# Performance work log

Hardware: AMD Instinct MI355X
Metric: run time of the kernel (lower is better)

The kernel has to match this reference:

```python
import jax, jax.numpy as jnp
import numpy as np

LATENT, CTX, HID, TDIM, HEADS = 512, 512, 1024, 128, 8
HEAD_DIM = HID // HEADS
SCALE = HEAD_DIM ** -0.5


def _ln(x, g, b, eps=1e-5):
    m = jnp.mean(x, axis=-1, keepdims=True)
    v = jnp.mean((x - m) ** 2, axis=-1, keepdims=True)
    return (x - m) * jax.lax.rsqrt(v + eps) * g + b


def _time_embed(t):
    half = TDIM // 2
    exponent = jnp.linspace(0.0, 1.0, half, dtype=t.dtype)
    freqs = jnp.exp(jnp.log(1000.0) * exponent)
    ang = 2.0 * jnp.pi * t[:, None] * freqs[None, :]
    return jnp.concatenate([jnp.sin(ang), jnp.cos(ang)], axis=-1)  # [B, TDIM]


def setup_inputs() -> dict:
    key = jax.random.key(0)
    ks = iter(jax.random.split(key, 32))
    B, M = 4096, 64

    def w(k, i, o):
        return jax.random.normal(k, (i, o), jnp.float32) * 0.02

    inp = {
        "states": jax.random.normal(next(ks), (B, LATENT), jnp.float32),
        "time_values": jax.random.uniform(next(ks), (B,), jnp.float32),
        "class_summary": jax.random.normal(next(ks), (B, CTX), jnp.float32),
        "support_memory": jax.random.normal(next(ks), (B, M, LATENT), jnp.float32),
        # state_trunk: LN(latent+tdim) -> Linear -> GELU -> Linear
        "trunk_ln_g": jnp.ones((LATENT + TDIM,)), "trunk_ln_b": jnp.zeros((LATENT + TDIM,)),
        "trunk_w1": w(next(ks), LATENT + TDIM, HID), "trunk_b1": jnp.zeros((HID,)),
        "trunk_w2": w(next(ks), HID, HID), "trunk_b2": jnp.zeros((HID,)),
        # memory adapter: LN(latent) -> Linear(latent, hid)
        "mem_ln_g": jnp.ones((LATENT,)), "mem_ln_b": jnp.zeros((LATENT,)),
        "mem_w": w(next(ks), LATENT, HID), "mem_b": jnp.zeros((HID,)),
        # attention projections
        "wq": w(next(ks), HID, HID), "bq": jnp.zeros((HID,)),
        "wk": w(next(ks), HID, HID), "bk": jnp.zeros((HID,)),
        "wv": w(next(ks), HID, HID), "bv": jnp.zeros((HID,)),
        "wo": w(next(ks), HID, HID), "bo": jnp.zeros((HID,)),
        # pre-condition norm + FiLM
        "pre_ln_g": jnp.ones((HID,)), "pre_ln_b": jnp.zeros((HID,)),
        "film_w": w(next(ks), CTX, 2 * HID), "film_b": jnp.zeros((2 * HID,)),
        # conditioner: LN -> Linear -> GELU -> Linear
        "cond_ln_g": jnp.ones((HID,)), "cond_ln_b": jnp.zeros((HID,)),
        "cond_w1": w(next(ks), HID, HID), "cond_b1": jnp.zeros((HID,)),
        "cond_w2": w(next(ks), HID, HID), "cond_b2": jnp.zeros((HID,)),
        # output head: LN -> Linear -> GELU -> Linear(hid, latent)
        "head_ln_g": jnp.ones((HID,)), "head_ln_b": jnp.zeros((HID,)),
        "head_w1": w(next(ks), HID, HID), "head_b1": jnp.zeros((HID,)),
        "head_w2": w(next(ks), HID, LATENT), "head_b2": jnp.zeros((LATENT,)),
    }
    return inp


def _forward(states, time_values, class_summary, support_memory,
             trunk_ln_g, trunk_ln_b, trunk_w1, trunk_b1, trunk_w2, trunk_b2,
             mem_ln_g, mem_ln_b, mem_w, mem_b,
             wq, bq, wk, bk, wv, bv, wo, bo,
             pre_ln_g, pre_ln_b, film_w, film_b,
             cond_ln_g, cond_ln_b, cond_w1, cond_b1, cond_w2, cond_b2,
             head_ln_g, head_ln_b, head_w1, head_b1, head_w2, head_b2):
    B, M, _ = support_memory.shape
    gelu = lambda x: jax.nn.gelu(x, approximate=False)

    # trunk: g = Trunk([y, gamma(t)])
    te = _time_embed(time_values)
    x = _ln(jnp.concatenate([states, te], axis=-1), trunk_ln_g, trunk_ln_b)
    g = gelu(x @ trunk_w1 + trunk_b1) @ trunk_w2 + trunk_b2  # [B, HID]

    # encode memory + single-query multi-head attention
    mem_h = _ln(support_memory, mem_ln_g, mem_ln_b) @ mem_w + mem_b  # [B, M, HID]
    q = (g @ wq + bq).reshape(B, HEADS, HEAD_DIM)
    k = (mem_h @ wk + bk).reshape(B, M, HEADS, HEAD_DIM)
    v = (mem_h @ wv + bv).reshape(B, M, HEADS, HEAD_DIM)
    logits = jnp.einsum("bhd,bmhd->bhm", q, k) * SCALE
    attn = jax.nn.softmax(logits, axis=-1)
    summary = jnp.einsum("bhm,bmhd->bhd", attn, v).reshape(B, HID)
    attn_summary = summary @ wo + bo

    # FiLM conditioning
    combined = _ln(g + attn_summary, pre_ln_g, pre_ln_b)
    film = class_summary @ film_w + film_b
    scale, shift = film[:, :HID], film[:, HID:]
    combined = (1.0 + scale) * combined + shift
    cond_x = _ln(combined, cond_ln_g, cond_ln_b)
    conditioned = gelu(cond_x @ cond_w1 + cond_b1) @ cond_w2 + cond_b2 + combined

    # output head
    hx = _ln(conditioned, head_ln_g, head_ln_b)
    return gelu(hx @ head_w1 + head_b1) @ head_w2 + head_b2  # [B, LATENT]


def reference(states, time_values, class_summary, support_memory,
              trunk_ln_g, trunk_ln_b, trunk_w1, trunk_b1, trunk_w2, trunk_b2,
              mem_ln_g, mem_ln_b, mem_w, mem_b,
              wq, bq, wk, bk, wv, bv, wo, bo,
              pre_ln_g, pre_ln_b, film_w, film_b,
              cond_ln_g, cond_ln_b, cond_w1, cond_b1, cond_w2, cond_b2,
              head_ln_g, head_ln_b, head_w1, head_b1, head_w2, head_b2):
    return _forward(states, time_values, class_summary, support_memory,
                    trunk_ln_g, trunk_ln_b, trunk_w1, trunk_b1, trunk_w2, trunk_b2,
                    mem_ln_g, mem_ln_b, mem_w, mem_b,
                    wq, bq, wk, bk, wv, bv, wo, bo,
                    pre_ln_g, pre_ln_b, film_w, film_b,
                    cond_ln_g, cond_ln_b, cond_w1, cond_b1, cond_w2, cond_b2,
                    head_ln_g, head_ln_b, head_w1, head_b1, head_w2, head_b2)
```

## Files before the change

### kernel.cpp

```cpp
#include <hip/hip_runtime.h>
#include <cstdint>
#include <cstddef>

typedef unsigned short ushort_t;
typedef short s16x8 __attribute__((ext_vector_type(8)));
typedef float f32x4 __attribute__((ext_vector_type(4)));

__device__ __forceinline__ float bf2f(ushort_t h){
  union { unsigned int u; float f; } v; v.u = ((unsigned int)h) << 16; return v.f;
}
__device__ __forceinline__ ushort_t f2bf(float x){
  union { float f; unsigned int u; } v; v.f = x;
  unsigned int r = v.u + 0x7FFFu + ((v.u >> 16) & 1u);
  return (ushort_t)(r >> 16);
}
__device__ __forceinline__ float gelu_f(float x){
  return 0.5f * x * (1.0f + erff(x * 0.7071067811865475f));
}
__device__ __forceinline__ float wave_sum(float v){
  #pragma unroll
  for (int o = 32; o; o >>= 1) v += __shfl_xor(v, o);
  return v;
}
__device__ __forceinline__ void block_reduce2(float& s, float& q, float* red){
  s = wave_sum(s); q = wave_sum(q);
  int w = threadIdx.x >> 6, lane = threadIdx.x & 63, nw = blockDim.x >> 6;
  if (lane == 0){ red[w] = s; red[8 + w] = q; }
  __syncthreads();
  float ts = 0.f, tq = 0.f;
  for (int i = 0; i < nw; ++i){ ts += red[i]; tq += red[8 + i]; }
  __syncthreads();
  s = ts; q = tq;
}

struct TDesc { const float* in; ushort_t* out; int K; int N; int start; };
struct PrepArgs {
  TDesc t[11];
  int ntiles_end;
  int cast1_blocks;
  int cast_end;
  const float* memw; ushort_t* memwb;
  const float* csum; ushort_t* csb;
  const float* memb; const float* wv; const float* bvp; float* bv2;
};

__global__ __launch_bounds__(256) void prep_k(PrepArgs a){
  int bid = blockIdx.x, tid = threadIdx.x;
  if (bid < a.ntiles_end){
    int d = 0;
    #pragma unroll
    for (int i = 1; i < 11; ++i) if (bid >= a.t[i].start) d = i;
    TDesc td = a.t[d];
    int tile = bid - td.start;
    int tilesx = td.N >> 5;
    int n0 = (tile % tilesx) << 5, k0 = (tile / tilesx) << 5;
    __shared__ float tbuf[32][33];
    int tx = tid & 31, ty = tid >> 5;
    #pragma unroll
    for (int j = 0; j < 32; j += 8)
      tbuf[ty + j][tx] = td.in[(size_t)(k0 + ty + j) * td.N + (n0 + tx)];
    __syncthreads();
    #pragma unroll
    for (int j = 0; j < 32; j += 8)
      td.out[(size_t)(n0 + ty + j) * td.K + (k0 + tx)] = f2bf(tbuf[tx][ty + j]);
  } else if (bid < a.cast_end){
    int ci = bid - a.ntiles_end;
    const float* src; ushort_t* dst; int i;
    if (ci < a.cast1_blocks){ src = a.memw; dst = a.memwb; i = ci * 1024 + tid * 4; }
    else { src = a.csum; dst = a.csb; i = (ci - a.cast1_blocks) * 1024 + tid * 4; }
    float4 v = *(const float4*)(src + i);
    union { ushort_t u[4]; uint2 p; } pk;
    pk.u[0] = f2bf(v.x); pk.u[1] = f2bf(v.y); pk.u[2] = f2bf(v.z); pk.u[3] = f2bf(v.w);
    *(uint2*)(dst + i) = pk.p;
  } else {
    int col = (bid - a.cast_end) * 256 + tid;
    float a0 = 0.f, a1 = 0.f, a2 = 0.f, a3 = 0.f;
    for (int j = 0; j < 1024; j += 4){
      a0 += a.memb[j + 0] * a.wv[(size_t)(j + 0) * 1024 + col];
      a1 += a.memb[j + 1] * a.wv[(size_t)(j + 1) * 1024 + col];
      a2 += a.memb[j + 2] * a.wv[(size_t)(j + 2) * 1024 + col];
      a3 += a.memb[j + 3] * a.wv[(size_t)(j + 3) * 1024 + col];
    }
    a.bv2[col] = a0 + a1 + a2 + a3 + a.bvp[col];
  }
}

__global__ __launch_bounds__(256) void ln_trunk_k(const float* __restrict__ states, const float* __restrict__ tv,
    const float* __restrict__ g, const float* __restrict__ b, ushort_t* __restrict__ out){
  int row = blockIdx.x, tid = threadIdx.x;
  __shared__ float buf[640];
  __shared__ float red[16];
  float t = tv[row];
  for (int i = tid; i < 640; i += 256){
    float v;
    if (i < 512) v = states[(size_t)row * 512 + i];
    else {
      int j = i - 512, jj = j & 63;
      float fr = expf(6.907755278982137f * ((float)jj * (1.0f / 63.0f)));
      float ang = 6.283185307179586f * t * fr;
      v = (j < 64) ? sinf(ang) : cosf(ang);
    }
    buf[i] = v;
  }
  __syncthreads();
  float s = 0.f, q = 0.f;
  for (int i = tid; i < 640; i += 256){ float v = buf[i]; s += v; q += v * v; }
  block_reduce2(s, q, red);
  float mean = s * (1.0f / 640.0f);
  float var = q * (1.0f / 640.0f) - mean * mean;
  float rstd = rsqrtf(var + 1e-5f);
  for (int i = tid; i < 640; i += 256)
    out[(size_t)row * 640 + i] = f2bf((buf[i] - mean) * rstd * g[i] + b[i]);
}

__global__ __launch_bounds__(256) void ln_rows_k(const float* __restrict__ in, const float* __restrict__ g,
    const float* __restrict__ b, ushort_t* __restrict__ out, int D){
  int row = blockIdx.x, tid = threadIdx.x, i = tid * 4;
  __shared__ float red[16];
  const float* x = in + (size_t)row * D;
  float4 v = *(const float4*)(x + i);
  float s = v.x + v.y + v.z + v.w;
  float q = v.x * v.x + v.y * v.y + v.z * v.z + v.w * v.w;
  block_reduce2(s, q, red);
  float invD = 1.0f / (float)D;
  float mean = s * invD, var = q * invD - mean * mean, rstd = rsqrtf(var + 1e-5f);
  union { ushort_t u[4]; uint2 p; } pk;
  pk.u[0] = f2bf((v.x - mean) * rstd * g[i + 0] + b[i + 0]);
  pk.u[1] = f2bf((v.y - mean) * rstd * g[i + 1] + b[i + 1]);
  pk.u[2] = f2bf((v.z - mean) * rstd * g[i + 2] + b[i + 2]);
  pk.u[3] = f2bf((v.w - mean) * rstd * g[i + 3] + b[i + 3]);
  *(uint2*)(out + (size_t)row * D + i) = pk.p;
}

__global__ __launch_bounds__(256) void fuse_film_k(const float* __restrict__ combf, const ushort_t* __restrict__ filmb,
    const float* __restrict__ pg, const float* __restrict__ pb,
    const float* __restrict__ cg, const float* __restrict__ cb,
    float* __restrict__ c2f, ushort_t* __restrict__ cxb){
  int row = blockIdx.x, tid = threadIdx.x, i = tid * 4;
  __shared__ float red[16];
  float4 a = *(const float4*)(combf + (size_t)row * 1024 + i);
  float x[4] = { a.x, a.y, a.z, a.w };
  float s = x[0] + x[1] + x[2] + x[3];
  float q = x[0]*x[0] + x[1]*x[1] + x[2]*x[2] + x[3]*x[3];
  block_reduce2(s, q, red);
  float mean = s * (1.0f / 1024.0f), var = q * (1.0f / 1024.0f) - mean * mean;
  float rstd = rsqrtf(var + 1e-5f);
  float4 pgv = *(const float4*)(pg + i), pbv = *(const float4*)(pb + i);
  union { uint2 p; ushort_t u[4]; } scv, shv;
  scv.p = *(const uint2*)(filmb + (size_t)row * 2048 + i);
  shv.p = *(const uint2*)(filmb + (size_t)row * 2048 + 1024 + i);
  float c2[4];
  {
    float pgx[4] = { pgv.x, pgv.y, pgv.z, pgv.w };
    float pbx[4] = { pbv.x, pbv.y, pbv.z, pbv.w };
    #pragma unroll
    for (int e = 0; e < 4; ++e){
      float cc = (x[e] - mean) * rstd * pgx[e] + pbx[e];
      c2[e] = (1.0f + bf2f(scv.u[e])) * cc + bf2f(shv.u[e]);
    }
  }
  *(float4*)(c2f + (size_t)row * 1024 + i) = make_float4(c2[0], c2[1], c2[2], c2[3]);
  float s2 = c2[0] + c2[1] + c2[2] + c2[3];
  float q2 = c2[0]*c2[0] + c2[1]*c2[1] + c2[2]*c2[2] + c2[3]*c2[3];
  block_reduce2(s2, q2, red);
  float m2 = s2 * (1.0f / 1024.0f), v2 = q2 * (1.0f / 1024.0f) - m2 * m2;
  float r2 = rsqrtf(v2 + 1e-5f);
  float4 cgv = *(const float4*)(cg + i), cbv = *(const float4*)(cb + i);
  union { ushort_t u[4]; uint2 p; } pk;
  pk.u[0] = f2bf((c2[0] - m2) * r2 * cgv.x + cbv.x);
  pk.u[1] = f2bf((c2[1] - m2) * r2 * cgv.y + cbv.y);
  pk.u[2] = f2bf((c2[2] - m2) * r2 * cgv.z + cbv.z);
  pk.u[3] = f2bf((c2[3] - m2) * r2 * cgv.w + cbv.w);
  *(uint2*)(cxb + (size_t)row * 1024 + i) = pk.p;
}

__global__ __launch_bounds__(256, 2) void suppattn_k(
    const float* __restrict__ support, const float* __restrict__ lgw, const float* __restrict__ lbw,
    const ushort_t* __restrict__ U, ushort_t* __restrict__ R)
{
  __shared__ ushort_t S[64 * 512];
  __shared__ ushort_t UG[9 * 512];
  __shared__ float WT[8][64];
  __shared__ float SUMV[64], SUMSQ[64];
  __shared__ __align__(16) float MEANR[64];
  __shared__ __align__(16) float RSTDR[64];
  __shared__ float PMAX[4][8], PSUM[4][8], PMU[4][8];
  __shared__ float AB[2][8];
  __shared__ float MUH[8];

  int bb = blockIdx.x, tid = threadIdx.x, w = tid >> 6, l = tid & 63;
  const ushort_t* Ub = U + (size_t)bb * 4096;

  for (int id = tid; id < 576; id += 256){
    int hr = id >> 6, cc = id & 63;
    int byteoff = hr * 1024 + (((cc & 56) | ((cc & 7) ^ (hr & 7))) << 4);
    uint4* dst = (uint4*)((char*)UG + byteoff);
    if (hr < 8){
      s16x8 uv = *(const s16x8*)(Ub + hr * 512 + cc * 8);
      float4 g0 = *(const float4*)(lgw + cc * 8);
      float4 g1 = *(const float4*)(lgw + cc * 8 + 4);
      float ga[8] = { g0.x, g0.y, g0.z, g0.w, g1.x, g1.y, g1.z, g1.w };
      union { ushort_t u[8]; uint4 p; } pk;
      #pragma unroll
      for (int e = 0; e < 8; ++e) pk.u[e] = f2bf(ga[e] * bf2f((ushort_t)uv[e]));
      *dst = pk.p;
    } else {
      *dst = make_uint4(0x3F803F80u, 0x3F803F80u, 0x3F803F80u, 0x3F803F80u);
    }
  }

  {
    int h0 = 2 * w, h1 = 2 * w + 1;
    s16x8 u0 = *(const s16x8*)(Ub + h0 * 512 + l * 8);
    s16x8 u1 = *(const s16x8*)(Ub + h1 * 512 + l * 8);
    float4 g0 = *(const float4*)(lgw + l * 8), g1 = *(const float4*)(lgw + l * 8 + 4);
    float4 c0 = *(const float4*)(lbw + l * 8), c1 = *(const float4*)(lbw + l * 8 + 4);
    float ga[8] = { g0.x, g0.y, g0.z, g0.w, g1.x, g1.y, g1.z, g1.w };
    float ba[8] = { c0.x, c0.y, c0.z, c0.w, c1.x, c1.y, c1.z, c1.w };
    float A0 = 0.f, B0 = 0.f, A1 = 0.f, B1 = 0.f;
    #pragma unroll
    for (int e = 0; e < 8; ++e){
      float x0 = bf2f((ushort_t)u0[e]), x1 = bf2f((ushort_t)u1[e]);
      A0 += ba[e] * x0; B0 += ga[e] * x0;
      A1 += ba[e] * x1; B1 += ga[e] * x1;
    }
    A0 = wave_sum(A0); B0 = wave_sum(B0); A1 = wave_sum(A1); B1 = wave_sum(B1);
    if (l == 0){ AB[0][h0] = A0; AB[1][h0] = B0; AB[0][h1] = A1; AB[1][h1] = B1; }
  }

  #pragma unroll 4
  for (int i = 0; i < 16; ++i){
    int m = i * 4 + w;
    const float* row = support + ((size_t)bb * 64 + m) * 512 + l * 8;
    float4 a0 = *(const float4*)row, a1 = *(const float4*)(row + 4);
    union { ushort_t u[8]; uint4 p; } pk;
    pk.u[0] = f2bf(a0.x); pk.u[1] = f2bf(a0.y); pk.u[2] = f2bf(a0.z); pk.u[3] = f2bf(a0.w);
    pk.u[4] = f2bf(a1.x); pk.u[5] = f2bf(a1.y); pk.u[6] = f2bf(a1.z); pk.u[7] = f2bf(a1.w);
    int byteoff = m * 1024 + (((l & 56) | ((l & 7) ^ (m & 7))) << 4);
    *(uint4*)((char*)S + byteoff) = pk.p;
  }
  __syncthreads();

  int l15 = l & 15, lk = l >> 4;
  int hr = (l15 < 8) ? l15 : 8;
  int arowb = (w * 16 + l15) * 1024;
  int hrowb = hr * 1024;
  f32x4 dacc = (f32x4){0.f, 0.f, 0.f, 0.f};
  f32x4 sacc = (f32x4){0.f, 0.f, 0.f, 0.f};
  #pragma unroll
  for (int ks = 0; ks < 16; ++ks){
    int cc = ks * 4 + lk;
    s16x8 afr = *(const s16x8*)((char*)S + arowb + (((cc & 56) | ((cc & 7) ^ (l15 & 7))) << 4));
    s16x8 bfr = *(const s16x8*)((char*)UG + hrowb + (((cc & 56) | ((cc & 7) ^ (hr & 7))) << 4));
    dacc = __builtin_amdgcn_mfma_f32_16x16x32_bf16(afr, bfr, dacc, 0, 0, 0);
    sacc = __builtin_amdgcn_mfma_f32_16x16x32_bf16(afr, afr, sacc, 0, 0, 0);
  }
  if (l15 == 8){
    #pragma unroll
    for (int j = 0; j < 4; ++j) SUMV[w * 16 + lk * 4 + j] = dacc[j];
  }
  if ((l15 >> 2) == lk) SUMSQ[w * 16 + l15] = sacc[l15 & 3];
  __syncthreads();
  if (tid < 64){
    float mean = SUMV[tid] * (1.0f / 512.0f);
    float var = SUMSQ[tid] * (1.0f / 512.0f) - mean * mean;
    MEANR[tid] = mean;
    RSTDR[tid] = rsqrtf(var + 1e-5f);
  }
  __syncthreads();

  int r0 = w * 16 + lk * 4;
  float4 mns = *(const float4*)(MEANR + r0);
  float4 rst = *(const float4*)(RSTDR + r0);
  float mn[4] = { mns.x, mns.y, mns.z, mns.w };
  float rs[4] = { rst.x, rst.y, rst.z, rst.w };
  float Ah = AB[0][l15 & 7], Bh = AB[1][l15 & 7];
  float lg[4];
  #pragma unroll
  for (int j = 0; j < 4; ++j)
    lg[j] = 0.08838834764831845f * (rs[j] * (dacc[j] - mn[j] * Bh) + Ah);
  float lmax = fmaxf(fmaxf(lg[0], lg[1]), fmaxf(lg[2], lg[3]));
  lmax = fmaxf(lmax, __shfl_xor(lmax, 16));
  lmax = fmaxf(lmax, __shfl_xor(lmax, 32));
  if (l < 8) PMAX[w][l] = lmax;
  __syncthreads();
  float gmax = fmaxf(fmaxf(PMAX[0][l15 & 7], PMAX[1][l15 & 7]),
                     fmaxf(PMAX[2][l15 & 7], PMAX[3][l15 & 7]));
  float e4[4]; float ls = 0.f, lm = 0.f;
  #pragma unroll
  for (int j = 0; j < 4; ++j){
    e4[j] = __expf(lg[j] - gmax);
    ls += e4[j];
    lm += e4[j] * rs[j] * mn[j];
  }
  ls += __shfl_xor(ls, 16); ls += __shfl_xor(ls, 32);
  lm += __shfl_xor(lm, 16); lm += __shfl_xor(lm, 32);
  if (l < 8){ PSUM[w][l] = ls; PMU[w][l] = lm; }
  __syncthreads();
  float Sh = PSUM[0][l15 & 7] + PSUM[1][l15 & 7] + PSUM[2][l15 & 7] + PSUM[3][l15 & 7];
  float inv = 1.0f / Sh;
  if (l15 < 8){
    #pragma unroll
    for (int j = 0; j < 4; ++j) WT[l15][r0 + j] = e4[j] * rs[j] * inv;
  }
  if (w == 0 && l < 8){
    MUH[l] = (PMU[0][l] + PMU[1][l] + PMU[2][l] + PMU[3][l]) * inv;
  }
  __syncthreads();

  int h0 = 2 * w, h1 = 2 * w + 1;
  float acc0[8] = {0.f,0.f,0.f,0.f,0.f,0.f,0.f,0.f};
  float acc1[8] = {0.f,0.f,0.f,0.f,0.f,0.f,0.f,0.f};
  #pragma unroll 4
  for (int m = 0; m < 64; ++m){
    s16x8 sv = *(const s16x8*)((char*)S + m * 1024 + (((l & 56) | ((l & 7) ^ (m & 7))) << 4));
    float f0 = WT[h0][m], f1 = WT[h1][m];
    #pragma unroll
    for (int e = 0; e < 8; ++e){
      float x = bf2f((ushort_t)sv[e]);
      acc0[e] += f0 * x;
      acc1[e] += f1 * x;
    }
  }
  {
    float4 g0 = *(const float4*)(lgw + l * 8), g1 = *(const float4*)(lgw + l * 8 + 4);
    float4 c0 = *(const float4*)(lbw + l * 8), c1 = *(const float4*)(lbw + l * 8 + 4);
    float ga[8] = { g0.x, g0.y, g0.z, g0.w, g1.x, g1.y, g1.z, g1.w };
    float ba[8] = { c0.x, c0.y, c0.z, c0.w, c1.x, c1.y, c1.z, c1.w };
    float mu0 = MUH[h0], mu1 = MUH[h1];
    union { ushort_t u[8]; uint4 p; } p0, p1;
    #pragma unroll
    for (int e = 0; e < 8; ++e){
      p0.u[e] = f2bf(ga[e] * (acc0[e] - mu0) + ba[e]);
      p1.u[e] = f2bf(ga[e] * (acc1[e] - mu1) + ba[e]);
    }
    *(uint4*)(R + (size_t)bb * 4096 + h0 * 512 + l * 8) = p0.p;
    *(uint4*)(R + (size_t)bb * 4096 + h1 * 512 + l * 8) = p1.p;
  }
}

#define GLL16(gsrc, ldst) \
  __builtin_amdgcn_global_load_lds((const __attribute__((address_space(1))) unsigned int*)(gsrc), \
                                   (__attribute__((address_space(3))) unsigned int*)(ldst), 16, 0, 0)

template<bool GELU, bool BIAS, bool WF32, bool WBF16, bool RESID>
__global__ __launch_bounds__(256, 3) void gemm_k(
    const ushort_t* __restrict__ A, int lda, long long aZ,
    const ushort_t* __restrict__ Bt, int ldb, long long bZ,
    const float* __restrict__ bias, long long biasZ,
    float* __restrict__ C, int ldc, long long cZ,
    ushort_t* __restrict__ Cb, int ldcb, long long cbZ,
    const float* __restrict__ R, int ldr,
    int M, int N, int K)
{
  __shared__ ushort_t smA[2][64 * 64];
  __shared__ ushort_t smB[2][128 * 64];
  int tid = threadIdx.x, lane = tid & 63, w = tid >> 6;
  int z = blockIdx.z;
  A  += (size_t)aZ * z;
  Bt += (size_t)bZ * z;
  if (BIAS)  bias += (size_t)biasZ * z;
  if (WF32)  C    += (size_t)cZ * z;
  if (WBF16) Cb   += (size_t)cbZ * z;

  int gx = gridDim.x, gy = gridDim.y;
  int nwg = gx * gy;
  int bx = blockIdx.x, by = blockIdx.y;
  if ((nwg & 7) == 0 && (gx & (gx - 1)) == 0){
    int lid = bx + gx * by;
    int cpx = nwg >> 3;
    int slid = (lid & 7) * cpx + (lid >> 3);
    int lgx = 31 - __clz(gx);
    bx = slid & (gx - 1);
    by = slid >> lgx;
  }
  int m0 = by * 64, n0 = bx * 128;
  int nk = K >> 6;

  auto stage = [&](int buf, int kt){
    int k0 = kt << 6;
    #pragma unroll
    for (int i = 0; i < 2; ++i){
      int c = ((w << 1) + i) * 64 + lane;
      int rowl = c >> 3, sp = c & 7;
      int sg = sp ^ (rowl & 7);
      GLL16(A + (size_t)(m0 + rowl) * lda + (k0 + sg * 8), &smA[buf][((w << 1) + i) * 512]);
    }
    #pragma unroll
    for (int i = 0; i < 4; ++i){
      int c = ((w << 2) + i) * 64 + lane;
      int rowl = c >> 3, sp = c & 7;
      int sg = sp ^ (rowl & 7);
      GLL16(Bt + (size_t)(n0 + rowl) * ldb + (k0 + sg * 8), &smB[buf][((w << 2) + i) * 512]);
    }
  };

  int qrow = w >> 1, qcol = w & 1;
  int l15 = lane & 15, lk = lane >> 4, l7 = lane & 7;
  int sb0 = ((0 + lk) ^ l7) << 4;
  int sb1 = ((4 + lk) ^ l7) << 4;
  int arow = (qrow * 32 + l15) * 128;
  int brow = (qcol * 64 + l15) * 128;

  f32x4 acc[2][4];
  #pragma unroll
  for (int m = 0; m < 2; ++m)
    #pragma unroll
    for (int n = 0; n < 4; ++n)
      acc[m][n] = (f32x4){0.f, 0.f, 0.f, 0.f};

  stage(0, 0);
  asm volatile("s_waitcnt vmcnt(0)" ::: "memory");
  __syncthreads();
  for (int kt = 0; kt < nk; ++kt){
    int cur = kt & 1;
    if (kt + 1 < nk) stage((kt + 1) & 1, kt + 1);
    const char* ab = (const char*)&smA[cur][0];
    const char* bbp = (const char*)&smB[cur][0];
    s16x8 af[2][2], bfv[4][2];
    #pragma unroll
    for (int m = 0; m < 2; ++m){
      af[m][0] = *(const s16x8*)(ab + arow + m * 2048 + sb0);
      af[m][1] = *(const s16x8*)(ab + arow + m * 2048 + sb1);
    }
    #pragma unroll
    for (int n = 0; n < 4; ++n){
      bfv[n][0] = *(const s16x8*)(bbp + brow + n * 2048 + sb0);
      bfv[n][1] = *(const s16x8*)(bbp + brow + n * 2048 + sb1);
    }
    #pragma unroll
    for (int kb = 0; kb < 2; ++kb)
      #pragma unroll
      for (int m = 0; m < 2; ++m)
        #pragma unroll
        for (int n = 0; n < 4; ++n)
          acc[m][n] = __builtin_amdgcn_mfma_f32_16x16x32_bf16(af[m][kb], bfv[n][kb], acc[m][n], 0, 0, 0);
    asm volatile("s_waitcnt vmcnt(0)" ::: "memory");
    __syncthreads();
  }

  #pragma unroll
  for (int n = 0; n < 4; ++n){
    int col = n0 + qcol * 64 + n * 16 + l15;
    float bvv = BIAS ? bias[col] : 0.0f;
    #pragma unroll
    for (int m = 0; m < 2; ++m){
      int rbase = m0 + qrow * 32 + m * 16 + lk * 4;
      #pragma unroll
      for (int r = 0; r < 4; ++r){
        float x = acc[m][n][r] + bvv;
        if (GELU) x = gelu_f(x);
        int row = rbase + r;
        if (RESID) x += R[(size_t)row * ldr + col];
        if (WF32)  C[(size_t)row * ldc + col] = x;
        if (WBF16) Cb[(size_t)row * ldcb + col] = f2bf(x);
      }
    }
  }
}

extern "C" void kernel_launch(void* const* d_in, const int* in_sizes, int n_in,
                              void* d_out, int out_size, void* d_ws, size_t ws_size,
                              hipStream_t stream)
{
  (void)in_sizes; (void)n_in; (void)out_size;
  const float* states      = (const float*)d_in[0];
  const float* time_values = (const float*)d_in[1];
  const float* class_sum   = (const float*)d_in[2];
  const float* support     = (const float*)d_in[3];
  const float* trunk_ln_g  = (const float*)d_in[4];
  const float* trunk_ln_b  = (const float*)d_in[5];
  const float* trunk_w1    = (const float*)d_in[6];
  const float* trunk_b1    = (const float*)d_in[7];
  const float* trunk_w2    = (const float*)d_in[8];
  const float* trunk_b2    = (const float*)d_in[9];
  const float* mem_ln_g    = (const float*)d_in[10];
  const float* mem_ln_b    = (const float*)d_in[11];
  const float* mem_w       = (const float*)d_in[12];
  const float* mem_b       = (const float*)d_in[13];
  const float* wq          = (const float*)d_in[14];
  const float* bq          = (const float*)d_in[15];
  const float* wk          = (const float*)d_in[16];
  const float* wv          = (const float*)d_in[18];
  const float* bvp         = (const float*)d_in[19];
  const float* wo          = (const float*)d_in[20];
  const float* bo          = (const float*)d_in[21];
  const float* pre_g       = (const float*)d_in[22];
  const float* pre_b       = (const float*)d_in[23];
  const float* film_w      = (const float*)d_in[24];
  const float* film_b      = (const float*)d_in[25];
  const float* cond_g      = (const float*)d_in[26];
  const float* cond_b      = (const float*)d_in[27];
  const float* cond_w1     = (const float*)d_in[28];
  const float* cond_b1     = (const float*)d_in[29];
  const float* cond_w2     = (const float*)d_in[30];
  const float* cond_b2     = (const float*)d_in[31];
  const float* head_g      = (const float*)d_in[32];
  const float* head_bb     = (const float*)d_in[33];
  const float* head_w1     = (const float*)d_in[34];
  const float* head_b1     = (const float*)d_in[35];
  const float* head_w2     = (const float*)d_in[36];
  const float* head_b2     = (const float*)d_in[37];
  float* out = (float*)d_out;

  char* ws = (char*)d_ws;
  size_t off = 0;
  auto alloc = [&](size_t bytes)->char*{
    char* p = ws + off;
    off += (bytes + 255) & ~(size_t)255;
    return p;
  };
  ushort_t* tw1T   = (ushort_t*)alloc((size_t)640 * 1024 * 2);
  ushort_t* tw2T   = (ushort_t*)alloc((size_t)1024 * 1024 * 2);
  ushort_t* wqT    = (ushort_t*)alloc((size_t)1024 * 1024 * 2);
  ushort_t* wkT    = (ushort_t*)alloc((size_t)1024 * 1024 * 2);
  ushort_t* wvT    = (ushort_t*)alloc((size_t)1024 * 1024 * 2);
  ushort_t* woT    = (ushort_t*)alloc((size_t)1024 * 1024 * 2);
  ushort_t* memw_b = (ushort_t*)alloc((size_t)512 * 1024 * 2);
  ushort_t* filmWT = (ushort_t*)alloc((size_t)512 * 2048 * 2);
  ushort_t* cw1T   = (ushort_t*)alloc((size_t)1024 * 1024 * 2);
  ushort_t* cw2T   = (ushort_t*)alloc((size_t)1024 * 1024 * 2);
  ushort_t* hw1T   = (ushort_t*)alloc((size_t)1024 * 1024 * 2);
  ushort_t* hw2T   = (ushort_t*)alloc((size_t)1024 * 512 * 2);
  ushort_t* K2     = (ushort_t*)alloc((size_t)512 * 1024 * 2);
  ushort_t* V2T    = (ushort_t*)alloc((size_t)1024 * 512 * 2);
  float*    bv2    = (float*)   alloc((size_t)1024 * 4);
  ushort_t* xnb    = (ushort_t*)alloc((size_t)4096 * 640 * 2);
  ushort_t* h1     = (ushort_t*)alloc((size_t)4096 * 1024 * 2);
  float*    gf     = (float*)   alloc((size_t)4096 * 1024 * 4);
  ushort_t* gb     = (ushort_t*)alloc((size_t)4096 * 1024 * 2);
  ushort_t* qb     = (ushort_t*)alloc((size_t)4096 * 1024 * 2);
  ushort_t* U      = (ushort_t*)alloc((size_t)4096 * 4096 * 2);
  ushort_t* Rb     = (ushort_t*)alloc((size_t)4096 * 4096 * 2);
  ushort_t* sumb   = (ushort_t*)alloc((size_t)4096 * 1024 * 2);
  float*    combf  = (float*)   alloc((size_t)4096 * 1024 * 4);
  ushort_t* csb    = (ushort_t*)alloc((size_t)4096 * 512 * 2);
  ushort_t* filmb  = (ushort_t*)alloc((size_t)4096 * 2048 * 2);
  float*    c2f    = (float*)   alloc((size_t)4096 * 1024 * 4);
  ushort_t* cxb    = (ushort_t*)alloc((size_t)4096 * 1024 * 2);
  ushort_t* c1     = (ushort_t*)alloc((size_t)4096 * 1024 * 2);
  float*    cond2f = (float*)   alloc((size_t)4096 * 1024 * 4);
  ushort_t* hxb    = (ushort_t*)alloc((size_t)4096 * 1024 * 2);
  ushort_t* h3     = (ushort_t*)alloc((size_t)4096 * 1024 * 2);
  if (off > ws_size) return;

  PrepArgs pa;
  int s = 0;
  auto setT = [&](int i, const float* in, ushort_t* o, int K, int N){
    pa.t[i].in = in; pa.t[i].out = o; pa.t[i].K = K; pa.t[i].N = N; pa.t[i].start = s;
    s += (N >> 5) * (K >> 5);
  };
  setT(0, trunk_w1, tw1T, 640, 1024);
  setT(1, trunk_w2, tw2T, 1024, 1024);
  setT(2, wq, wqT, 1024, 1024);
  setT(3, wk, wkT, 1024, 1024);
  setT(4, wv, wvT, 1024, 1024);
  setT(5, wo, woT, 1024, 1024);
  setT(6, film_w, filmWT, 512, 2048);
  setT(7, cond_w1, cw1T, 1024, 1024);
  setT(8, cond_w2, cw2T, 1024, 1024);
  setT(9, head_w1, hw1T, 1024, 1024);
  setT(10, head_w2, hw2T, 1024, 512);
  pa.ntiles_end = s;
  pa.cast1_blocks = (512 * 1024) / 1024;
  pa.cast_end = s + pa.cast1_blocks + (4096 * 512) / 1024;
  pa.memw = mem_w; pa.memwb = memw_b;
  pa.csum = class_sum; pa.csb = csb;
  pa.memb = mem_b; pa.wv = wv; pa.bvp = bvp; pa.bv2 = bv2;
  prep_k<<<pa.cast_end + 4, 256, 0, stream>>>(pa);

  gemm_k<false, false, false, true, false><<<dim3(8, 8, 1), 256, 0, stream>>>(
      memw_b, 1024, 0, wkT, 1024, 0, nullptr, 0, nullptr, 0, 0, K2, 1024, 0, nullptr, 0, 512, 1024, 1024);
  gemm_k<false, false, false, true, false><<<dim3(4, 16, 1), 256, 0, stream>>>(
      wvT, 1024, 0, memw_b, 1024, 0, nullptr, 0, nullptr, 0, 0, V2T, 512, 0, nullptr, 0, 1024, 512, 1024);

  ln_trunk_k<<<4096, 256, 0, stream>>>(states, time_values, trunk_ln_g, trunk_ln_b, xnb);
  gemm_k<true, true, false, true, false><<<dim3(8, 64, 1), 256, 0, stream>>>(
      xnb, 640, 0, tw1T, 640, 0, trunk_b1, 0, nullptr, 0, 0, h1, 1024, 0, nullptr, 0, 4096, 1024, 640);
  gemm_k<false, true, true, true, false><<<dim3(8, 64, 1), 256, 0, stream>>>(
      h1, 1024, 0, tw2T, 1024, 0, trunk_b2, 0, gf, 1024, 0, gb, 1024, 0, nullptr, 0, 4096, 1024, 1024);
  gemm_k<false, true, false, true, false><<<dim3(8, 64, 1), 256, 0, stream>>>(
      gb, 1024, 0, wqT, 1024, 0, bq, 0, nullptr, 0, 0, qb, 1024, 0, nullptr, 0, 4096, 1024, 1024);
  gemm_k<false, false, false, true, false><<<dim3(4, 64, 8), 256, 0, stream>>>(
      qb, 1024, 128, K2, 1024, 128, nullptr, 0, nullptr, 0, 0, U, 4096, 512, nullptr, 0, 4096, 512, 128);

  suppattn_k<<<4096, 256, 0, stream>>>(support, mem_ln_g, mem_ln_b, U, Rb);

  gemm_k<false, true, false, true, false><<<dim3(1, 64, 8), 256, 0, stream>>>(
      Rb, 4096, 512, V2T, 512, 65536, bv2, 128, nullptr, 0, 0, sumb, 1024, 128, nullptr, 0, 4096, 128, 512);

  gemm_k<false, true, true, false, true><<<dim3(8, 64, 1), 256, 0, stream>>>(
      sumb, 1024, 0, woT, 1024, 0, bo, 0, combf, 1024, 0, nullptr, 0, 0, gf, 1024, 4096, 1024, 1024);
  gemm_k<false, true, false, true, false><<<dim3(16, 64, 1), 256, 0, stream>>>(
      csb, 512, 0, filmWT, 512, 0, film_b, 0, nullptr, 0, 0, filmb, 2048, 0, nullptr, 0, 4096, 2048, 512);

  fuse_film_k<<<4096, 256, 0, stream>>>(combf, filmb, pre_g, pre_b, cond_g, cond_b, c2f, cxb);

  gemm_k<true, true, false, true, false><<<dim3(8, 64, 1), 256, 0, stream>>>(
      cxb, 1024, 0, cw1T, 1024, 0, cond_b1, 0, nullptr, 0, 0, c1, 1024, 0, nullptr, 0, 4096, 1024, 1024);
  gemm_k<false, true, true, false, true><<<dim3(8, 64, 1), 256, 0, stream>>>(
      c1, 1024, 0, cw2T, 1024, 0, cond_b2, 0, cond2f, 1024, 0, nullptr, 0, 0, c2f, 1024, 4096, 1024, 1024);
  ln_rows_k<<<4096, 256, 0, stream>>>(cond2f, head_g, head_bb, hxb, 1024);
  gemm_k<true, true, false, true, false><<<dim3(8, 64, 1), 256, 0, stream>>>(
      hxb, 1024, 0, hw1T, 1024, 0, head_b1, 0, nullptr, 0, 0, h3, 1024, 0, nullptr, 0, 4096, 1024, 1024);
  gemm_k<false, true, true, false, false><<<dim3(4, 64, 1), 256, 0, stream>>>(
      h3, 1024, 0, hw2T, 1024, 0, head_b2, 0, out, 512, 0, nullptr, 0, 0, nullptr, 0, 4096, 512, 1024);
}
```

Before: 469.6 us.

## Store residual activations in bf16, fuse trunk LN into prep, MFMA support aggregation

Residual and intermediate activations (trunk output, attention combine, FiLM output, conditioner output) are now stored and read as bf16 rather than fp32, halving their memory traffic and removing duplicate fp32 buffers. The trunk LayerNorm kernel is merged into the prep kernel as extra blocks, saving one launch. In the support-attention kernel, the weighted sum over memory slots is recomputed with MFMA bf16 instructions instead of scalar FMAs, using a modified swizzle. Quantizing the residual stream and the attention weights to bf16 lowers accuracy.

```diff
diff --git a/kernel.cpp b/kernel.cpp
--- a/kernel.cpp
+++ b/kernel.cpp
@@ -33,8 +33,11 @@
   s = ts; q = tq;
 }
 
+#define SSLOT(cc, m) (((cc) & 56) | (((cc) & 7) ^ (((m) ^ ((m) >> 3)) & 7)))
+
 struct TDesc { const float* in; ushort_t* out; int K; int N; int start; };
 struct PrepArgs {
+  const float* states; const float* tv; const float* lng; const float* lnb; ushort_t* xnb;
   TDesc t[11];
   int ntiles_end;
   int cast1_blocks;
@@ -46,6 +49,35 @@
 
 __global__ __launch_bounds__(256) void prep_k(PrepArgs a){
   int bid = blockIdx.x, tid = threadIdx.x;
+  __shared__ float buf[640];
+  __shared__ float red[16];
+  __shared__ float tbuf[32][33];
+  if (bid < 4096){
+    int row = bid;
+    float t = a.tv[row];
+    for (int i = tid; i < 640; i += 256){
+      float v;
+      if (i < 512) v = a.states[(size_t)row * 512 + i];
+      else {
+        int j = i - 512, jj = j & 63;
+        float fr = expf(6.907755278982137f * ((float)jj * (1.0f / 63.0f)));
+        float ang = 6.283185307179586f * t * fr;
+        v = (j < 64) ? sinf(ang) : cosf(ang);
+      }
+      buf[i] = v;
+    }
+    __syncthreads();
+    float s = 0.f, q = 0.f;
+    for (int i = tid; i < 640; i += 256){ float v = buf[i]; s += v; q += v * v; }
+    block_reduce2(s, q, red);
+    float mean = s * (1.0f / 640.0f);
+    float var = q * (1.0f / 640.0f) - mean * mean;
+    float rstd = rsqrtf(var + 1e-5f);
+    for (int i = tid; i < 640; i += 256)
+      a.xnb[(size_t)row * 640 + i] = f2bf((buf[i] - mean) * rstd * a.lng[i] + a.lnb[i]);
+    return;
+  }
+  bid -= 4096;
   if (bid < a.ntiles_end){
     int d = 0;
     #pragma unroll
@@ -54,7 +86,6 @@
     int tile = bid - td.start;
     int tilesx = td.N >> 5;
     int n0 = (tile % tilesx) << 5, k0 = (tile / tilesx) << 5;
-    __shared__ float tbuf[32][33];
     int tx = tid & 31, ty = tid >> 5;
     #pragma unroll
     for (int j = 0; j < 32; j += 8)
@@ -85,61 +116,33 @@
   }
 }
 
-__global__ __launch_bounds__(256) void ln_trunk_k(const float* __restrict__ states, const float* __restrict__ tv,
-    const float* __restrict__ g, const float* __restrict__ b, ushort_t* __restrict__ out){
-  int row = blockIdx.x, tid = threadIdx.x;
-  __shared__ float buf[640];
-  __shared__ float red[16];
-  float t = tv[row];
-  for (int i = tid; i < 640; i += 256){
-    float v;
-    if (i < 512) v = states[(size_t)row * 512 + i];
-    else {
-      int j = i - 512, jj = j & 63;
-      float fr = expf(6.907755278982137f * ((float)jj * (1.0f / 63.0f)));
-      float ang = 6.283185307179586f * t * fr;
-      v = (j < 64) ? sinf(ang) : cosf(ang);
-    }
-    buf[i] = v;
-  }
-  __syncthreads();
-  float s = 0.f, q = 0.f;
-  for (int i = tid; i < 640; i += 256){ float v = buf[i]; s += v; q += v * v; }
-  block_reduce2(s, q, red);
-  float mean = s * (1.0f / 640.0f);
-  float var = q * (1.0f / 640.0f) - mean * mean;
-  float rstd = rsqrtf(var + 1e-5f);
-  for (int i = tid; i < 640; i += 256)
-    out[(size_t)row * 640 + i] = f2bf((buf[i] - mean) * rstd * g[i] + b[i]);
-}
-
-__global__ __launch_bounds__(256) void ln_rows_k(const float* __restrict__ in, const float* __restrict__ g,
+__global__ __launch_bounds__(256) void ln_rows_k(const ushort_t* __restrict__ in, const float* __restrict__ g,
     const float* __restrict__ b, ushort_t* __restrict__ out, int D){
   int row = blockIdx.x, tid = threadIdx.x, i = tid * 4;
   __shared__ float red[16];
-  const float* x = in + (size_t)row * D;
-  float4 v = *(const float4*)(x + i);
-  float s = v.x + v.y + v.z + v.w;
-  float q = v.x * v.x + v.y * v.y + v.z * v.z + v.w * v.w;
+  union { uint2 p; ushort_t u[4]; } vv;
+  vv.p = *(const uint2*)(in + (size_t)row * D + i);
+  float v[4] = { bf2f(vv.u[0]), bf2f(vv.u[1]), bf2f(vv.u[2]), bf2f(vv.u[3]) };
+  float s = v[0] + v[1] + v[2] + v[3];
+  float q = v[0]*v[0] + v[1]*v[1] + v[2]*v[2] + v[3]*v[3];
   block_reduce2(s, q, red);
   float invD = 1.0f / (float)D;
   float mean = s * invD, var = q * invD - mean * mean, rstd = rsqrtf(var + 1e-5f);
   union { ushort_t u[4]; uint2 p; } pk;
-  pk.u[0] = f2bf((v.x - mean) * rstd * g[i + 0] + b[i + 0]);
-  pk.u[1] = f2bf((v.y - mean) * rstd * g[i + 1] + b[i + 1]);
-  pk.u[2] = f2bf((v.z - mean) * rstd * g[i + 2] + b[i + 2]);
-  pk.u[3] = f2bf((v.w - mean) * rstd * g[i + 3] + b[i + 3]);
+  #pragma unroll
+  for (int e = 0; e < 4; ++e) pk.u[e] = f2bf((v[e] - mean) * rstd * g[i + e] + b[i + e]);
   *(uint2*)(out + (size_t)row * D + i) = pk.p;
 }
 
-__global__ __launch_bounds__(256) void fuse_film_k(const float* __restrict__ combf, const ushort_t* __restrict__ filmb,
+__global__ __launch_bounds__(256) void fuse_film_k(const ushort_t* __restrict__ combb, const ushort_t* __restrict__ filmb,
     const float* __restrict__ pg, const float* __restrict__ pb,
     const float* __restrict__ cg, const float* __restrict__ cb,
-    float* __restrict__ c2f, ushort_t* __restrict__ cxb){
+    ushort_t* __restrict__ c2b, ushort_t* __restrict__ cxb){
   int row = blockIdx.x, tid = threadIdx.x, i = tid * 4;
   __shared__ float red[16];
-  float4 a = *(const float4*)(combf + (size_t)row * 1024 + i);
-  float x[4] = { a.x, a.y, a.z, a.w };
+  union { uint2 p; ushort_t u[4]; } av;
+  av.p = *(const uint2*)(combb + (size_t)row * 1024 + i);
+  float x[4] = { bf2f(av.u[0]), bf2f(av.u[1]), bf2f(av.u[2]), bf2f(av.u[3]) };
   float s = x[0] + x[1] + x[2] + x[3];
   float q = x[0]*x[0] + x[1]*x[1] + x[2]*x[2] + x[3]*x[3];
   block_reduce2(s, q, red);
@@ -159,7 +162,10 @@
       c2[e] = (1.0f + bf2f(scv.u[e])) * cc + bf2f(shv.u[e]);
     }
   }
-  *(float4*)(c2f + (size_t)row * 1024 + i) = make_float4(c2[0], c2[1], c2[2], c2[3]);
+  union { ushort_t u[4]; uint2 p; } pc;
+  #pragma unroll
+  for (int e = 0; e < 4; ++e) pc.u[e] = f2bf(c2[e]);
+  *(uint2*)(c2b + (size_t)row * 1024 + i) = pc.p;
   float s2 = c2[0] + c2[1] + c2[2] + c2[3];
   float q2 = c2[0]*c2[0] + c2[1]*c2[1] + c2[2]*c2[2] + c2[3]*c2[3];
   block_reduce2(s2, q2, red);
@@ -180,7 +186,7 @@
 {
   __shared__ ushort_t S[64 * 512];
   __shared__ ushort_t UG[9 * 512];
-  __shared__ float WT[8][64];
+  __shared__ float WTf[8][65];
   __shared__ float SUMV[64], SUMSQ[64];
   __shared__ __align__(16) float MEANR[64];
   __shared__ __align__(16) float RSTDR[64];
@@ -192,11 +198,11 @@
   const ushort_t* Ub = U + (size_t)bb * 4096;
 
   for (int id = tid; id < 576; id += 256){
-    int hr = id >> 6, cc = id & 63;
-    int byteoff = hr * 1024 + (((cc & 56) | ((cc & 7) ^ (hr & 7))) << 4);
+    int hr8 = id >> 6, cc = id & 63;
+    int byteoff = hr8 * 1024 + (((cc & 56) | ((cc & 7) ^ (hr8 & 7))) << 4);
     uint4* dst = (uint4*)((char*)UG + byteoff);
-    if (hr < 8){
-      s16x8 uv = *(const s16x8*)(Ub + hr * 512 + cc * 8);
+    if (hr8 < 8){
+      s16x8 uv = *(const s16x8*)(Ub + hr8 * 512 + cc * 8);
       float4 g0 = *(const float4*)(lgw + cc * 8);
       float4 g1 = *(const float4*)(lgw + cc * 8 + 4);
       float ga[8] = { g0.x, g0.y, g0.z, g0.w, g1.x, g1.y, g1.z, g1.w };
@@ -236,7 +242,7 @@
     union { ushort_t u[8]; uint4 p; } pk;
     pk.u[0] = f2bf(a0.x); pk.u[1] = f2bf(a0.y); pk.u[2] = f2bf(a0.z); pk.u[3] = f2bf(a0.w);
     pk.u[4] = f2bf(a1.x); pk.u[5] = f2bf(a1.y); pk.u[6] = f2bf(a1.z); pk.u[7] = f2bf(a1.w);
-    int byteoff = m * 1024 + (((l & 56) | ((l & 7) ^ (m & 7))) << 4);
+    int byteoff = m * 1024 + (SSLOT(l, m) << 4);
     *(uint4*)((char*)S + byteoff) = pk.p;
   }
   __syncthreads();
@@ -245,12 +251,13 @@
   int hr = (l15 < 8) ? l15 : 8;
   int arowb = (w * 16 + l15) * 1024;
   int hrowb = hr * 1024;
+  int am = w * 16 + l15;
   f32x4 dacc = (f32x4){0.f, 0.f, 0.f, 0.f};
   f32x4 sacc = (f32x4){0.f, 0.f, 0.f, 0.f};
   #pragma unroll
   for (int ks = 0; ks < 16; ++ks){
     int cc = ks * 4 + lk;
-    s16x8 afr = *(const s16x8*)((char*)S + arowb + (((cc & 56) | ((cc & 7) ^ (l15 & 7))) << 4));
+    s16x8 afr = *(const s16x8*)((char*)S + arowb + (SSLOT(cc, am) << 4));
     s16x8 bfr = *(const s16x8*)((char*)UG + hrowb + (((cc & 56) | ((cc & 7) ^ (hr & 7))) << 4));
     dacc = __builtin_amdgcn_mfma_f32_16x16x32_bf16(afr, bfr, dacc, 0, 0, 0);
     sacc = __builtin_amdgcn_mfma_f32_16x16x32_bf16(afr, afr, sacc, 0, 0, 0);
@@ -301,41 +308,52 @@
   float inv = 1.0f / Sh;
   if (l15 < 8){
     #pragma unroll
-    for (int j = 0; j < 4; ++j) WT[l15][r0 + j] = e4[j] * rs[j] * inv;
+    for (int j = 0; j < 4; ++j) WTf[l15][r0 + j] = e4[j] * rs[j] * inv;
   }
   if (w == 0 && l < 8){
     MUH[l] = (PMU[0][l] + PMU[1][l] + PMU[2][l] + PMU[3][l]) * inv;
   }
   __syncthreads();
 
-  int h0 = 2 * w, h1 = 2 * w + 1;
-  float acc0[8] = {0.f,0.f,0.f,0.f,0.f,0.f,0.f,0.f};
-  float acc1[8] = {0.f,0.f,0.f,0.f,0.f,0.f,0.f,0.f};
-  #pragma unroll 4
-  for (int m = 0; m < 64; ++m){
-    s16x8 sv = *(const s16x8*)((char*)S + m * 1024 + (((l & 56) | ((l & 7) ^ (m & 7))) << 4));
-    float f0 = WT[h0][m], f1 = WT[h1][m];
+  union { ushort_t u[8]; s16x8 v; } af0, af1;
+  af0.v = (s16x8){0,0,0,0,0,0,0,0};
+  af1.v = (s16x8){0,0,0,0,0,0,0,0};
+  if (l15 < 8){
     #pragma unroll
     for (int e = 0; e < 8; ++e){
-      float x = bf2f((ushort_t)sv[e]);
-      acc0[e] += f0 * x;
-      acc1[e] += f1 * x;
-    }
-  }
-  {
-    float4 g0 = *(const float4*)(lgw + l * 8), g1 = *(const float4*)(lgw + l * 8 + 4);
-    float4 c0 = *(const float4*)(lbw + l * 8), c1 = *(const float4*)(lbw + l * 8 + 4);
-    float ga[8] = { g0.x, g0.y, g0.z, g0.w, g1.x, g1.y, g1.z, g1.w };
-    float ba[8] = { c0.x, c0.y, c0.z, c0.w, c1.x, c1.y, c1.z, c1.w };
-    float mu0 = MUH[h0], mu1 = MUH[h1];
-    union { ushort_t u[8]; uint4 p; } p0, p1;
+      af0.u[e] = f2bf(WTf[l15][lk * 8 + e]);
+      af1.u[e] = f2bf(WTf[l15][32 + lk * 8 + e]);
+    }
+  }
+  float mu[4];
+  #pragma unroll
+  for (int j = 0; j < 4; ++j) mu[j] = (lk < 2) ? MUH[lk * 4 + j] : 0.f;
+
+  const char* Sp = (const char*)S;
+  #pragma unroll
+  for (int ns = 0; ns < 8; ++ns){
+    int c = w * 128 + ns * 16 + l15;
+    int cch = c >> 3, cb = (c & 7) * 2;
+    int sb = cch & 56, cl = cch & 7;
+    union { ushort_t u[8]; s16x8 v; } bf0, bf1;
     #pragma unroll
     for (int e = 0; e < 8; ++e){
-      p0.u[e] = f2bf(ga[e] * (acc0[e] - mu0) + ba[e]);
-      p1.u[e] = f2bf(ga[e] * (acc1[e] - mu1) + ba[e]);
-    }
-    *(uint4*)(R + (size_t)bb * 4096 + h0 * 512 + l * 8) = p0.p;
-    *(uint4*)(R + (size_t)bb * 4096 + h1 * 512 + l * 8) = p1.p;
+      int m0 = lk * 8 + e;
+      int m1 = m0 + 32;
+      bf0.u[e] = *(const ushort_t*)(Sp + m0 * 1024 + ((sb | (cl ^ ((m0 ^ lk) & 7))) << 4) + cb);
+      bf1.u[e] = *(const ushort_t*)(Sp + m1 * 1024 + ((sb | (cl ^ ((m1 ^ (4 + lk)) & 7))) << 4) + cb);
+    }
+    f32x4 cacc = (f32x4){0.f, 0.f, 0.f, 0.f};
+    cacc = __builtin_amdgcn_mfma_f32_16x16x32_bf16(af0.v, bf0.v, cacc, 0, 0, 0);
+    cacc = __builtin_amdgcn_mfma_f32_16x16x32_bf16(af1.v, bf1.v, cacc, 0, 0, 0);
+    if (lk < 2){
+      float gc = lgw[c], bc = lbw[c];
+      #pragma unroll
+      for (int j = 0; j < 4; ++j){
+        int h = lk * 4 + j;
+        R[(size_t)bb * 4096 + h * 512 + c] = f2bf(gc * (cacc[j] - mu[j]) + bc);
+      }
+    }
   }
 }
 
@@ -350,7 +368,7 @@
     const float* __restrict__ bias, long long biasZ,
     float* __restrict__ C, int ldc, long long cZ,
     ushort_t* __restrict__ Cb, int ldcb, long long cbZ,
-    const float* __restrict__ R, int ldr,
+    const ushort_t* __restrict__ R, int ldr,
     int M, int N, int K)
 {
   __shared__ ushort_t smA[2][64 * 64];
@@ -451,7 +469,7 @@
         float x = acc[m][n][r] + bvv;
         if (GELU) x = gelu_f(x);
         int row = rbase + r;
-        if (RESID) x += R[(size_t)row * ldr + col];
+        if (RESID) x += bf2f(R[(size_t)row * ldr + col]);
         if (WF32)  C[(size_t)row * ldc + col] = x;
         if (WBF16) Cb[(size_t)row * ldcb + col] = f2bf(x);
       }
@@ -527,24 +545,24 @@
   float*    bv2    = (float*)   alloc((size_t)1024 * 4);
   ushort_t* xnb    = (ushort_t*)alloc((size_t)4096 * 640 * 2);
   ushort_t* h1     = (ushort_t*)alloc((size_t)4096 * 1024 * 2);
-  float*    gf     = (float*)   alloc((size_t)4096 * 1024 * 4);
   ushort_t* gb     = (ushort_t*)alloc((size_t)4096 * 1024 * 2);
   ushort_t* qb     = (ushort_t*)alloc((size_t)4096 * 1024 * 2);
   ushort_t* U      = (ushort_t*)alloc((size_t)4096 * 4096 * 2);
   ushort_t* Rb     = (ushort_t*)alloc((size_t)4096 * 4096 * 2);
   ushort_t* sumb   = (ushort_t*)alloc((size_t)4096 * 1024 * 2);
-  float*    combf  = (float*)   alloc((size_t)4096 * 1024 * 4);
+  ushort_t* combb  = (ushort_t*)alloc((size_t)4096 * 1024 * 2);
   ushort_t* csb    = (ushort_t*)alloc((size_t)4096 * 512 * 2);
   ushort_t* filmb  = (ushort_t*)alloc((size_t)4096 * 2048 * 2);
-  float*    c2f    = (float*)   alloc((size_t)4096 * 1024 * 4);
+  ushort_t* c2b    = (ushort_t*)alloc((size_t)4096 * 1024 * 2);
   ushort_t* cxb    = (ushort_t*)alloc((size_t)4096 * 1024 * 2);
   ushort_t* c1     = (ushort_t*)alloc((size_t)4096 * 1024 * 2);
-  float*    cond2f = (float*)   alloc((size_t)4096 * 1024 * 4);
+  ushort_t* cond2b = (ushort_t*)alloc((size_t)4096 * 1024 * 2);
   ushort_t* hxb    = (ushort_t*)alloc((size_t)4096 * 1024 * 2);
   ushort_t* h3     = (ushort_t*)alloc((size_t)4096 * 1024 * 2);
   if (off > ws_size) return;
 
   PrepArgs pa;
+  pa.states = states; pa.tv = time_values; pa.lng = trunk_ln_g; pa.lnb = trunk_ln_b; pa.xnb = xnb;
   int s = 0;
   auto setT = [&](int i, const float* in, ushort_t* o, int K, int N){
     pa.t[i].in = in; pa.t[i].out = o; pa.t[i].K = K; pa.t[i].N = N; pa.t[i].start = s;
@@ -567,18 +585,17 @@
   pa.memw = mem_w; pa.memwb = memw_b;
   pa.csum = class_sum; pa.csb = csb;
   pa.memb = mem_b; pa.wv = wv; pa.bvp = bvp; pa.bv2 = bv2;
-  prep_k<<<pa.cast_end + 4, 256, 0, stream>>>(pa);
+  prep_k<<<4096 + pa.cast_end + 4, 256, 0, stream>>>(pa);
 
   gemm_k<false, false, false, true, false><<<dim3(8, 8, 1), 256, 0, stream>>>(
       memw_b, 1024, 0, wkT, 1024, 0, nullptr, 0, nullptr, 0, 0, K2, 1024, 0, nullptr, 0, 512, 1024, 1024);
   gemm_k<false, false, false, true, false><<<dim3(4, 16, 1), 256, 0, stream>>>(
       wvT, 1024, 0, memw_b, 1024, 0, nullptr, 0, nullptr, 0, 0, V2T, 512, 0, nullptr, 0, 1024, 512, 1024);
 
-  ln_trunk_k<<<4096, 256, 0, stream>>>(states, time_values, trunk_ln_g, trunk_ln_b, xnb);
   gemm_k<true, true, false, true, false><<<dim3(8, 64, 1), 256, 0, stream>>>(
       xnb, 640, 0, tw1T, 640, 0, trunk_b1, 0, nullptr, 0, 0, h1, 1024, 0, nullptr, 0, 4096, 1024, 640);
-  gemm_k<false, true, true, true, false><<<dim3(8, 64, 1), 256, 0, stream>>>(
-      h1, 1024, 0, tw2T, 1024, 0, trunk_b2, 0, gf, 1024, 0, gb, 1024, 0, nullptr, 0, 4096, 1024, 1024);
+  gemm_k<false, true, false, true, false><<<dim3(8, 64, 1), 256, 0, stream>>>(
+      h1, 1024, 0, tw2T, 1024, 0, trunk_b2, 0, nullptr, 0, 0, gb, 1024, 0, nullptr, 0, 4096, 1024, 1024);
   gemm_k<false, true, false, true, false><<<dim3(8, 64, 1), 256, 0, stream>>>(
       gb, 1024, 0, wqT, 1024, 0, bq, 0, nullptr, 0, 0, qb, 1024, 0, nullptr, 0, 4096, 1024, 1024);
   gemm_k<false, false, false, true, false><<<dim3(4, 64, 8), 256, 0, stream>>>(
@@ -589,18 +606,18 @@
   gemm_k<false, true, false, true, false><<<dim3(1, 64, 8), 256, 0, stream>>>(
       Rb, 4096, 512, V2T, 512, 65536, bv2, 128, nullptr, 0, 0, sumb, 1024, 128, nullptr, 0, 4096, 128, 512);
 
-  gemm_k<false, true, true, false, true><<<dim3(8, 64, 1), 256, 0, stream>>>(
-      sumb, 1024, 0, woT, 1024, 0, bo, 0, combf, 1024, 0, nullptr, 0, 0, gf, 1024, 4096, 1024, 1024);
+  gemm_k<false, true, false, true, true><<<dim3(8, 64, 1), 256, 0, stream>>>(
+      sumb, 1024, 0, woT, 1024, 0, bo, 0, nullptr, 0, 0, combb, 1024, 0, gb, 1024, 4096, 1024, 1024);
   gemm_k<false, true, false, true, false><<<dim3(16, 64, 1), 256, 0, stream>>>(
       csb, 512, 0, filmWT, 512, 0, film_b, 0, nullptr, 0, 0, filmb, 2048, 0, nullptr, 0, 4096, 2048, 512);
 
-  fuse_film_k<<<4096, 256, 0, stream>>>(combf, filmb, pre_g, pre_b, cond_g, cond_b, c2f, cxb);
+  fuse_film_k<<<4096, 256, 0, stream>>>(combb, filmb, pre_g, pre_b, cond_g, cond_b, c2b, cxb);
 
   gemm_k<true, true, false, true, false><<<dim3(8, 64, 1), 256, 0, stream>>>(
       cxb, 1024, 0, cw1T, 1024, 0, cond_b1, 0, nullptr, 0, 0, c1, 1024, 0, nullptr, 0, 4096, 1024, 1024);
-  gemm_k<false, true, true, false, true><<<dim3(8, 64, 1), 256, 0, stream>>>(
-      c1, 1024, 0, cw2T, 1024, 0, cond_b2, 0, cond2f, 1024, 0, nullptr, 0, 0, c2f, 1024, 4096, 1024, 1024);
-  ln_rows_k<<<4096, 256, 0, stream>>>(cond2f, head_g, head_bb, hxb, 1024);
+  gemm_k<false, true, false, true, true><<<dim3(8, 64, 1), 256, 0, stream>>>(
+      c1, 1024, 0, cw2T, 1024, 0, cond_b2, 0, nullptr, 0, 0, cond2b, 1024, 0, c2b, 1024, 4096, 1024, 1024);
+  ln_rows_k<<<4096, 256, 0, stream>>>(cond2b, head_g, head_bb, hxb, 1024);
   gemm_k<true, true, false, true, false><<<dim3(8, 64, 1), 256, 0, stream>>>(
       hxb, 1024, 0, hw1T, 1024, 0, head_b1, 0, nullptr, 0, 0, h3, 1024, 0, nullptr, 0, 4096, 1024, 1024);
   gemm_k<false, true, true, false, false><<<dim3(4, 64, 1), 256, 0, stream>>>(
```

Result: faster. 451.8 us (-3.8%).
